# Optimization experiments

Hardware: AMD Instinct MI355X
Metric: run time of the kernel (lower is better)

The kernel has to match this reference:

```python
import math
from itertools import product
import jax, jax.numpy as jnp
import numpy as np

# ---- static config (mirrors LPD.__init__) ----
IMG_W, IMG_H = 1920, 1080
MIN_SIZES = [[10, 16, 24], [32, 48], [64, 96], [128, 192, 256]]
STEPS = [8, 16, 32, 64]
VARIANCE = (0.1, 0.2)
CONF_THR = 0.3
NMS_THR = 0.3
TOP_K = 2000
KEEP_TOP_K = 750
BATCH = 16


def make_priors() -> np.ndarray:
    """Anchor grid in normalized (cx, cy, w, h), kornia _PriorBox order:
    per level, per cell (row-major), per min_size."""
    levels = []
    for step, mss in zip(STEPS, MIN_SIZES):
        fh, fw = math.ceil(IMG_H / step), math.ceil(IMG_W / step)
        ii, jj = np.meshgrid(np.arange(fh), np.arange(fw), indexing='ij')
        cx = (jj + 0.5) * step / IMG_W  # [fh, fw]
        cy = (ii + 0.5) * step / IMG_H
        nms_ = len(mss)
        cx = np.broadcast_to(cx[..., None], (fh, fw, nms_))
        cy = np.broadcast_to(cy[..., None], (fh, fw, nms_))
        skx = np.broadcast_to(np.array(mss, np.float64) / IMG_W, (fh, fw, nms_))
        sky = np.broadcast_to(np.array(mss, np.float64) / IMG_H, (fh, fw, nms_))
        levels.append(np.stack([cx, cy, skx, sky], -1).reshape(-1, 4))
    return np.concatenate(levels, 0).astype(np.float32)  # [N, 4]

N_PRIORS = make_priors().shape[0]  # 119130 for 1920x1080


def decode(loc, priors):
    """loc [B,N,14], priors [N,4] -> scaled [B,N,14] (x1y1x2y2 + 5 landmarks)."""
    var = jnp.asarray(VARIANCE, loc.dtype)
    p_xy, p_wh = priors[:, :2], priors[:, 2:4]
    cxcy = p_xy + loc[..., 0:2] * VARIANCE[0] * p_wh
    wh = p_wh * jnp.exp(loc[..., 2:4] * var)
    x1y1 = cxcy - wh * 0.5
    x2y2 = x1y1 + wh
    # 5 landmark points
    lmk = p_xy[None, :, None, :] + loc[..., 4:14].reshape(*loc.shape[:-1], 5, 2) * VARIANCE[0] * p_wh[None, :, None, :]
    boxes = jnp.concatenate([x1y1, x2y2, lmk.reshape(*loc.shape[:-1], 10)], -1)
    scale = jnp.tile(jnp.asarray([IMG_W, IMG_H], loc.dtype), 7)
    return boxes * scale


def nms_keep(b, s):
    """Greedy NMS. b [K,4] sorted by descending score s [K]. Returns bool keep [K]."""
    area = jnp.clip(b[:, 2] - b[:, 0], 0.0) * jnp.clip(b[:, 3] - b[:, 1], 0.0)
    lt = jnp.maximum(b[:, None, :2], b[None, :, :2])
    rb = jnp.minimum(b[:, None, 2:4], b[None, :, 2:4])
    whi = jnp.clip(rb - lt, 0.0)
    inter = whi[..., 0] * whi[..., 1]
    iou_m = inter / (area[:, None] + area[None, :] - inter + 1e-9)  # [K,K]
    K = b.shape[0]
    idx = jnp.arange(K)

    def step(active, i):
        keep_i = active[i]
        active = active & ~(keep_i & (iou_m[i] > NMS_THR) & (idx > i))
        return active, keep_i

    _, keep = jax.lax.scan(step, s > 0.0, idx)
    return keep


def setup_inputs() -> dict:
    key = jax.random.key(0)
    k1, k2, k3 = jax.random.split(key, 3)
    return {
        'loc': jax.random.normal(k1, (BATCH, N_PRIORS, 14), jnp.float32),
        'conf': jax.random.normal(k2, (BATCH, N_PRIORS, 2), jnp.float32),
        'iou': jax.random.normal(k3, (BATCH, N_PRIORS, 1), jnp.float32),
    }


def reference(loc, conf, iou):
    priors = jnp.asarray(make_priors())  # [N,4] constant
    cls = jax.nn.softmax(conf, axis=-1)[..., 1]          # [B,N]
    iou_s = jnp.clip(iou[..., 0], 0.0, 1.0)
    scores = jnp.sqrt(cls * iou_s)
    scores = jnp.where(scores >= CONF_THR, scores, 0.0)  # confidence threshold
    boxes = decode(loc, priors)                          # [B,N,14]
    top_s, top_i = jax.lax.top_k(scores, TOP_K)          # sorted desc
    boxes_k = jnp.take_along_axis(boxes, top_i[..., None], axis=1)  # [B,K,14]
    keep = jax.vmap(nms_keep)(boxes_k[..., :4], top_s)   # [B,K] bool
    keep = keep & (jnp.cumsum(keep.astype(jnp.int32), axis=-1) <= KEEP_TOP_K)
    dets = jnp.concatenate([boxes_k, (top_s * keep)[..., None]], -1)  # [B,K,15]
    return dets
```

## Files before the change

### kernel.cpp

```cpp
#include <hip/hip_runtime.h>
#include <math.h>

#define BB 16
#define TOPK 2000
#define KEEPK 750
#define CAND_CAP 4096
#define EDGE_CAP 8192
#define HIST_BINS 256
#define BIN_BASE 0x3E99u

#define OFF_HIST   0
#define OFF_CCOUNT 16384
#define OFF_ECOUNT 16448
#define ZERO_BYTES 16512
#define OFF_SBITS  16512

__global__ __launch_bounds__(256) void k_scores(const float* __restrict__ conf,
                                                const float* __restrict__ iou,
                                                unsigned* __restrict__ sbits,
                                                unsigned* __restrict__ hist, int N) {
  __shared__ unsigned h[HIST_BINS];
  int b = blockIdx.y;
  for (int i = threadIdx.x; i < HIST_BINS; i += blockDim.x) h[i] = 0;
  __syncthreads();
  const float2* c2 = (const float2*)conf + (size_t)b * N;
  const float* iu = iou + (size_t)b * N;
  unsigned* sb = sbits + (size_t)b * N;
  int n0 = blockIdx.x * 4096;
#pragma unroll 4
  for (int k = 0; k < 16; ++k) {
    int n = n0 + k * 256 + threadIdx.x;
    if (n < N) {
      float2 c = c2[n];
      float m = fmaxf(c.x, c.y);
      float e0 = (float)exp((double)(c.x - m));
      float e1 = (float)exp((double)(c.y - m));
      float p1 = e1 / (e0 + e1);
      float ic = fminf(fmaxf(iu[n], 0.0f), 1.0f);
      float s = sqrtf(p1 * ic);
      s = (s >= 0.3f) ? s : 0.0f;
      unsigned bits = __float_as_uint(s);
      sb[n] = bits;
      if (bits != 0u) {
        int bin = (int)(bits >> 16) - (int)BIN_BASE;
        bin = bin < 0 ? 0 : (bin > 255 ? 255 : bin);
        atomicAdd(&h[bin], 1u);
      }
    }
  }
  __syncthreads();
  for (int i = threadIdx.x; i < HIST_BINS; i += blockDim.x)
    if (h[i]) atomicAdd(&hist[b * HIST_BINS + i], h[i]);
}

__global__ __launch_bounds__(256) void k_compact(const unsigned* __restrict__ sbits,
                                                 const unsigned* __restrict__ hist,
                                                 unsigned* __restrict__ ccount,
                                                 unsigned long long* __restrict__ ckeys,
                                                 int N) {
  __shared__ unsigned sT;
  __shared__ unsigned long long masks[32];
  __shared__ unsigned wioff[32];
  __shared__ unsigned blockbase;
  int b = blockIdx.y;
  int tid = threadIdx.x, lane = tid & 63, wv = tid >> 6;

  if (tid < 64) {
    const unsigned* h = hist + b * HIST_BINS;
    unsigned v0 = h[255 - (4 * lane + 0)];
    unsigned v1 = h[255 - (4 * lane + 1)];
    unsigned v2 = h[255 - (4 * lane + 2)];
    unsigned v3 = h[255 - (4 * lane + 3)];
    unsigned p0 = v0, p1 = p0 + v1, p2 = p1 + v2, p3 = p2 + v3;
    unsigned tot = p3, pre = tot;
    for (int off = 1; off < 64; off <<= 1) {
      unsigned q = __shfl_up(pre, off);
      if (lane >= off) pre += q;
    }
    unsigned excl = pre - tot;
    int kk = -1;
    if (excl + p0 >= TOPK) kk = 0;
    else if (excl + p1 >= TOPK) kk = 1;
    else if (excl + p2 >= TOPK) kk = 2;
    else if (excl + p3 >= TOPK) kk = 3;
    unsigned long long m = __ballot(kk >= 0);
    int bin = 0;
    if (m != 0ull) {
      int fl = __ffsll((unsigned long long)m) - 1;
      int fk = __shfl(kk, fl);
      bin = 255 - (4 * fl + fk);
    }
    if (lane == 0) sT = ((unsigned)(BIN_BASE + (unsigned)bin)) << 16;
  }
  __syncthreads();
  unsigned T = sT;

  const unsigned* sb = sbits + (size_t)b * N;
  int n0 = blockIdx.x * 2048;
  unsigned v[8];
  unsigned long long mk[8];
#pragma unroll
  for (int k = 0; k < 8; ++k) {
    int n = n0 + k * 256 + tid;
    v[k] = (n < N) ? sb[n] : 0u;
    bool p = v[k] >= T;
    mk[k] = __ballot(p);
    if (lane == 0) masks[k * 4 + wv] = mk[k];
  }
  __syncthreads();
  if (tid < 64) {
    unsigned c = (tid < 32) ? (unsigned)__popcll(masks[tid]) : 0u;
    unsigned pre = c;
    for (int off = 1; off < 64; off <<= 1) {
      unsigned q = __shfl_up(pre, off);
      if (lane >= off) pre += q;
    }
    if (tid < 32) wioff[tid] = pre - c;
    if (tid == 31) blockbase = atomicAdd(&ccount[b], pre);
  }
  __syncthreads();
  unsigned base = blockbase;
#pragma unroll
  for (int k = 0; k < 8; ++k) {
    if ((mk[k] >> lane) & 1ull) {
      unsigned pos = base + wioff[k * 4 + wv] +
                     (unsigned)__popcll(mk[k] & ((1ull << lane) - 1ull));
      if (pos < CAND_CAP) {
        int n = n0 + k * 256 + tid;
        ckeys[(size_t)b * CAND_CAP + pos] =
            ((unsigned long long)v[k] << 32) | (unsigned)(~(unsigned)n);
      }
    }
  }
}

__global__ __launch_bounds__(1024) void k_sort(const unsigned* __restrict__ ccount,
                                               const unsigned long long* __restrict__ ckeys,
                                               float* __restrict__ top_s,
                                               unsigned* __restrict__ top_i) {
  __shared__ unsigned long long s[CAND_CAP];
  int b = blockIdx.x;
  unsigned c = ccount[b];
  if (c > CAND_CAP) c = CAND_CAP;
  for (int i = threadIdx.x; i < CAND_CAP; i += 1024)
    s[i] = (i < (int)c) ? ckeys[(size_t)b * CAND_CAP + i] : 0ull;
  __syncthreads();
  for (int k = 2; k <= CAND_CAP; k <<= 1) {
    for (int j = k >> 1; j > 0; j >>= 1) {
      for (int i = threadIdx.x; i < CAND_CAP; i += 1024) {
        int p = i ^ j;
        if (p > i) {
          bool up = (i & k) == 0;
          unsigned long long a = s[i], bb2 = s[p];
          bool sw = up ? (a < bb2) : (a > bb2);
          if (sw) { s[i] = bb2; s[p] = a; }
        }
      }
      __syncthreads();
    }
  }
  for (int r = threadIdx.x; r < TOPK; r += 1024) {
    unsigned long long key = s[r];
    top_s[b * TOPK + r] = __uint_as_float((unsigned)(key >> 32));
    top_i[b * TOPK + r] = ~(unsigned)key;
  }
}

__global__ __launch_bounds__(256) void k_decode(const float* __restrict__ loc,
                                                const unsigned* __restrict__ top_i,
                                                float* __restrict__ out,
                                                float4* __restrict__ boxes4, int N) {
  int r = blockIdx.x * blockDim.x + threadIdx.x;
  int b = blockIdx.y;
  if (r >= TOPK) return;
  unsigned idxu = top_i[b * TOPK + r];
  if (idxu >= (unsigned)N) idxu = 0;
  int i = (int)idxu;
  int off, fw, st, nm, lvl;
  if (i < 97200)       { lvl = 0; off = 0;      fw = 240; st = 8;  nm = 3; }
  else if (i < 113520) { lvl = 1; off = 97200;  fw = 120; st = 16; nm = 2; }
  else if (i < 117600) { lvl = 2; off = 113520; fw = 60;  st = 32; nm = 2; }
  else                 { lvl = 3; off = 117600; fw = 30;  st = 64; nm = 3; }
  int t = i - off;
  int cell = t / nm;
  int k = t - cell * nm;
  int row = cell / fw;
  int col = cell - row * fw;
  int msv = (lvl == 0) ? (k == 0 ? 10 : (k == 1 ? 16 : 24))
          : (lvl == 1) ? (k == 0 ? 32 : 48)
          : (lvl == 2) ? (k == 0 ? 64 : 96)
                       : (k == 0 ? 128 : (k == 1 ? 192 : 256));
  float cx  = (float)(((double)col + 0.5) * (double)st / 1920.0);
  float cy  = (float)(((double)row + 0.5) * (double)st / 1080.0);
  float skx = (float)((double)msv / 1920.0);
  float sky = (float)((double)msv / 1080.0);
  const float2* lp2 = (const float2*)(loc + ((size_t)b * N + (size_t)i) * 14);
  float l[14];
#pragma unroll
  for (int q = 0; q < 7; ++q) { float2 v = lp2[q]; l[2 * q] = v.x; l[2 * q + 1] = v.y; }
  float cx2 = cx + (l[0] * 0.1f) * skx;
  float cy2 = cy + (l[1] * 0.1f) * sky;
  float wx = skx * expf(l[2] * 0.1f);
  float wy = sky * expf(l[3] * 0.2f);
  float x1 = cx2 - wx * 0.5f, y1 = cy2 - wy * 0.5f;
  float x2 = x1 + wx, y2 = y1 + wy;
  float X1 = x1 * 1920.0f, Y1 = y1 * 1080.0f, X2 = x2 * 1920.0f, Y2 = y2 * 1080.0f;
  float* o = out + ((size_t)b * TOPK + r) * 15;
  o[0] = X1; o[1] = Y1; o[2] = X2; o[3] = Y2;
#pragma unroll
  for (int q = 0; q < 5; ++q) {
    o[4 + 2 * q] = (cx + (l[4 + 2 * q] * 0.1f) * skx) * 1920.0f;
    o[5 + 2 * q] = (cy + (l[5 + 2 * q] * 0.1f) * sky) * 1080.0f;
  }
  boxes4[b * TOPK + r] = make_float4(X1, Y1, X2, Y2);
}

__global__ __launch_bounds__(256) void k_edges(const float4* __restrict__ boxes4,
                                               unsigned* __restrict__ ecount,
                                               unsigned* __restrict__ edges) {
  __shared__ float4 cb[256];
  __shared__ unsigned loc_e[1024];
  __shared__ unsigned lcnt, gbase;
  int b = blockIdx.y;
  int t = blockIdx.x;
  int ib = 0;
  while ((ib + 1) * (ib + 2) / 2 <= t) ++ib;
  int jb = t - ib * (ib + 1) / 2;
  int tid = threadIdx.x;
  if (tid == 0) lcnt = 0;
  int j0 = jb * 256;
  {
    int j = j0 + tid;
    cb[tid] = (j < TOPK) ? boxes4[b * TOPK + j]
                         : make_float4(-1e30f, -1e30f, -1e30f, -1e30f);
  }
  __syncthreads();
  int r = ib * 256 + tid;
  bool valid = r < TOPK;
  float4 A = valid ? boxes4[b * TOPK + r] : make_float4(0, 0, 0, 0);
  float areaA = fmaxf(A.z - A.x, 0.f) * fmaxf(A.w - A.y, 0.f);
  int cmax = r - j0;
  if (cmax > 256) cmax = 256;
  if (!valid) cmax = 0;
  for (int c = 0; c < cmax; ++c) {
    float4 Bx = cb[c];
    float xx1 = fmaxf(A.x, Bx.x), yy1 = fmaxf(A.y, Bx.y);
    float xx2 = fminf(A.z, Bx.z), yy2 = fminf(A.w, Bx.w);
    float w = fmaxf(xx2 - xx1, 0.f), hgt = fmaxf(yy2 - yy1, 0.f);
    float inter = w * hgt;
    float areaB = fmaxf(Bx.z - Bx.x, 0.f) * fmaxf(Bx.w - Bx.y, 0.f);
    float iouv = inter / (areaA + areaB - inter + 1e-9f);
    if (iouv > 0.3f) {
      unsigned p = atomicAdd(&lcnt, 1u);
      if (p < 1024u) loc_e[p] = ((unsigned)r << 16) | (unsigned)(j0 + c);
    }
  }
  __syncthreads();
  unsigned cnt = lcnt;
  if (cnt > 1024u) cnt = 1024u;
  if (tid == 0 && cnt) gbase = atomicAdd(&ecount[b], cnt);
  __syncthreads();
  if (cnt)
    for (unsigned e = tid; e < cnt; e += 256) {
      unsigned p = gbase + e;
      if (p < EDGE_CAP) edges[b * EDGE_CAP + p] = loc_e[e];
    }
}

__global__ __launch_bounds__(256) void k_nms(const float* __restrict__ top_s,
                                             const unsigned* __restrict__ ecount,
                                             const unsigned* __restrict__ edges,
                                             float* __restrict__ out) {
  int b = blockIdx.x;
  __shared__ unsigned long long A[32], K[32], S[32];
  __shared__ unsigned pref[32];
  __shared__ unsigned ecache[2048];
  __shared__ int changed;
  int tid = threadIdx.x, lane = tid & 63, wv = tid >> 6;
  for (int base = 0; base < 2048; base += 256) {
    int i = base + tid;
    bool act = (i < TOPK) && (top_s[b * TOPK + i] > 0.0f);
    unsigned long long m = __ballot(act);
    if (lane == 0) { int w = (base >> 6) + wv; A[w] = m; K[w] = m; }
  }
  unsigned E = ecount[b];
  if (E > EDGE_CAP) E = EDGE_CAP;
  unsigned Ec = E > 2048u ? 2048u : E;
  for (unsigned e = tid; e < Ec; e += 256) ecache[e] = edges[b * EDGE_CAP + e];
  __syncthreads();
  for (int it = 0; it < 32; ++it) {
    if (tid == 0) changed = 0;
    if (tid < 32) S[tid] = 0ull;
    __syncthreads();
    for (unsigned e = tid; e < Ec; e += 256) {
      unsigned v = ecache[e];
      unsigned i = v >> 16, j = v & 0xFFFFu;
      if ((K[j >> 6] >> (j & 63)) & 1ull) atomicOr(&S[i >> 6], 1ull << (i & 63));
    }
    for (unsigned e = 2048u + tid; e < E; e += 256) {
      unsigned v = edges[b * EDGE_CAP + e];
      unsigned i = v >> 16, j = v & 0xFFFFu;
      if ((K[j >> 6] >> (j & 63)) & 1ull) atomicOr(&S[i >> 6], 1ull << (i & 63));
    }
    __syncthreads();
    if (tid < 32) {
      unsigned long long nk = A[tid] & ~S[tid];
      if (nk != K[tid]) { K[tid] = nk; changed = 1; }
    }
    __syncthreads();
    if (!changed) break;
  }
  if (tid == 0) {
    unsigned acc = 0;
    for (int w = 0; w < 32; ++w) { pref[w] = acc; acc += (unsigned)__popcll(K[w]); }
  }
  __syncthreads();
  for (int base = 0; base < 2048; base += 256) {
    int i = base + tid;
    if (i < TOPK) {
      int w = i >> 6;
      unsigned long long bit = (K[w] >> (i & 63)) & 1ull;
      unsigned rank = pref[w] + (unsigned)__popcll(K[w] & ((1ull << (i & 63)) - 1ull)) +
                      (unsigned)bit;
      float sv = top_s[b * TOPK + i];
      out[((size_t)b * TOPK + i) * 15 + 14] = (bit && rank <= KEEPK) ? sv : 0.0f;
    }
  }
}

extern "C" void kernel_launch(void* const* d_in, const int* in_sizes, int n_in,
                              void* d_out, int out_size, void* d_ws, size_t ws_size,
                              hipStream_t stream) {
  const float* loc  = (const float*)d_in[0];
  const float* conf = (const float*)d_in[1];
  const float* iou  = (const float*)d_in[2];
  float* out = (float*)d_out;
  int N = in_sizes[2] / BB;

  char* ws = (char*)d_ws;
  unsigned* hist   = (unsigned*)(ws + OFF_HIST);
  unsigned* ccount = (unsigned*)(ws + OFF_CCOUNT);
  unsigned* ecount = (unsigned*)(ws + OFF_ECOUNT);
  unsigned* sbits  = (unsigned*)(ws + OFF_SBITS);
  size_t off = (size_t)OFF_SBITS + (size_t)BB * N * 4;
  off = (off + 15) & ~(size_t)15;
  unsigned long long* ckeys = (unsigned long long*)(ws + off); off += (size_t)BB * CAND_CAP * 8;
  float*    top_s = (float*)(ws + off);    off += (size_t)BB * TOPK * 4;
  unsigned* top_i = (unsigned*)(ws + off); off += (size_t)BB * TOPK * 4;
  off = (off + 15) & ~(size_t)15;
  float4* boxes4 = (float4*)(ws + off);    off += (size_t)BB * TOPK * 16;
  unsigned* edges = (unsigned*)(ws + off); off += (size_t)BB * EDGE_CAP * 4;

  hipMemsetAsync(ws, 0, ZERO_BYTES, stream);

  k_scores<<<dim3((N + 4095) / 4096, BB), 256, 0, stream>>>(conf, iou, sbits, hist, N);
  k_compact<<<dim3((N + 2047) / 2048, BB), 256, 0, stream>>>(sbits, hist, ccount, ckeys, N);
  k_sort<<<BB, 1024, 0, stream>>>(ccount, ckeys, top_s, top_i);
  k_decode<<<dim3((TOPK + 255) / 256, BB), 256, 0, stream>>>(loc, top_i, out, boxes4, N);
  k_edges<<<dim3(36, BB), 256, 0, stream>>>(boxes4, ecount, edges);
  k_nms<<<BB, 256, 0, stream>>>(top_s, ecount, edges, out);
}
```

Measured before the change: 296.8 us.

## Register-resident bitonic sort with wavefront shuffles, fused with box decode

Rewrites the per-batch bitonic sort so each thread holds four keys in registers. In-thread compares handle strides below 4 and wavefront XOR shuffles handle strides up to 64 wide in thread space, so shared memory and block barriers are used only for the large strides. The decode step is fused into the sort kernel, which removes one kernel launch and the top_i round trip through global memory. In exchange, decode now runs on only 500 threads per batch across 16 blocks, so the gathers from loc are less parallel.

```diff
diff --git a/kernel.cpp b/kernel.cpp
--- a/kernel.cpp
+++ b/kernel.cpp
@@ -134,85 +134,115 @@
   }
 }
 
-__global__ __launch_bounds__(1024) void k_sort(const unsigned* __restrict__ ccount,
-                                               const unsigned long long* __restrict__ ckeys,
-                                               float* __restrict__ top_s,
-                                               unsigned* __restrict__ top_i) {
+__global__ __launch_bounds__(1024) void k_sort_decode(
+    const unsigned* __restrict__ ccount, const unsigned long long* __restrict__ ckeys,
+    const float* __restrict__ loc, float* __restrict__ top_s,
+    float* __restrict__ out, float4* __restrict__ boxes4, int N) {
   __shared__ unsigned long long s[CAND_CAP];
   int b = blockIdx.x;
+  int t = threadIdx.x;
   unsigned c = ccount[b];
   if (c > CAND_CAP) c = CAND_CAP;
-  for (int i = threadIdx.x; i < CAND_CAP; i += 1024)
-    s[i] = (i < (int)c) ? ckeys[(size_t)b * CAND_CAP + i] : 0ull;
-  __syncthreads();
+  const unsigned long long* src = ckeys + (size_t)b * CAND_CAP;
+  unsigned long long key[4];
+#pragma unroll
+  for (int e = 0; e < 4; ++e) {
+    int i = 4 * t + e;
+    key[e] = (i < (int)c) ? src[i] : 0ull;
+  }
   for (int k = 2; k <= CAND_CAP; k <<= 1) {
     for (int j = k >> 1; j > 0; j >>= 1) {
-      for (int i = threadIdx.x; i < CAND_CAP; i += 1024) {
-        int p = i ^ j;
-        if (p > i) {
-          bool up = (i & k) == 0;
-          unsigned long long a = s[i], bb2 = s[p];
-          bool sw = up ? (a < bb2) : (a > bb2);
-          if (sw) { s[i] = bb2; s[p] = a; }
+      if (j >= 256) {
+        __syncthreads();
+#pragma unroll
+        for (int e = 0; e < 4; ++e) s[4 * t + e] = key[e];
+        __syncthreads();
+        int pbase = (4 * t) ^ j;
+        bool own_lo = ((4 * t) & j) == 0;
+        bool dir = ((4 * t) & k) == 0;
+        bool keep_max = (own_lo == dir);
+#pragma unroll
+        for (int e = 0; e < 4; ++e) {
+          unsigned long long o = s[pbase + e];
+          unsigned long long mx = key[e] > o ? key[e] : o;
+          unsigned long long mn = key[e] > o ? o : key[e];
+          key[e] = keep_max ? mx : mn;
+        }
+      } else if (j >= 4) {
+        int d = j >> 2;
+        bool own_lo = (t & d) == 0;
+        bool dir = ((4 * t) & k) == 0;
+        bool keep_max = (own_lo == dir);
+#pragma unroll
+        for (int e = 0; e < 4; ++e) {
+          unsigned long long o = __shfl_xor(key[e], d, 64);
+          unsigned long long mx = key[e] > o ? key[e] : o;
+          unsigned long long mn = key[e] > o ? o : key[e];
+          key[e] = keep_max ? mx : mn;
+        }
+      } else {
+#pragma unroll
+        for (int e = 0; e < 4; ++e) {
+          int p = e ^ j;
+          if (p > e) {
+            int i = 4 * t + e;
+            bool dir = ((i & k) == 0);
+            bool need = dir ? (key[e] < key[p]) : (key[e] > key[p]);
+            if (need) { unsigned long long tmp = key[e]; key[e] = key[p]; key[p] = tmp; }
+          }
         }
       }
-      __syncthreads();
-    }
-  }
-  for (int r = threadIdx.x; r < TOPK; r += 1024) {
-    unsigned long long key = s[r];
-    top_s[b * TOPK + r] = __uint_as_float((unsigned)(key >> 32));
-    top_i[b * TOPK + r] = ~(unsigned)key;
-  }
-}
-
-__global__ __launch_bounds__(256) void k_decode(const float* __restrict__ loc,
-                                                const unsigned* __restrict__ top_i,
-                                                float* __restrict__ out,
-                                                float4* __restrict__ boxes4, int N) {
-  int r = blockIdx.x * blockDim.x + threadIdx.x;
-  int b = blockIdx.y;
-  if (r >= TOPK) return;
-  unsigned idxu = top_i[b * TOPK + r];
-  if (idxu >= (unsigned)N) idxu = 0;
-  int i = (int)idxu;
-  int off, fw, st, nm, lvl;
-  if (i < 97200)       { lvl = 0; off = 0;      fw = 240; st = 8;  nm = 3; }
-  else if (i < 113520) { lvl = 1; off = 97200;  fw = 120; st = 16; nm = 2; }
-  else if (i < 117600) { lvl = 2; off = 113520; fw = 60;  st = 32; nm = 2; }
-  else                 { lvl = 3; off = 117600; fw = 30;  st = 64; nm = 3; }
-  int t = i - off;
-  int cell = t / nm;
-  int k = t - cell * nm;
-  int row = cell / fw;
-  int col = cell - row * fw;
-  int msv = (lvl == 0) ? (k == 0 ? 10 : (k == 1 ? 16 : 24))
-          : (lvl == 1) ? (k == 0 ? 32 : 48)
-          : (lvl == 2) ? (k == 0 ? 64 : 96)
-                       : (k == 0 ? 128 : (k == 1 ? 192 : 256));
-  float cx  = (float)(((double)col + 0.5) * (double)st / 1920.0);
-  float cy  = (float)(((double)row + 0.5) * (double)st / 1080.0);
-  float skx = (float)((double)msv / 1920.0);
-  float sky = (float)((double)msv / 1080.0);
-  const float2* lp2 = (const float2*)(loc + ((size_t)b * N + (size_t)i) * 14);
-  float l[14];
-#pragma unroll
-  for (int q = 0; q < 7; ++q) { float2 v = lp2[q]; l[2 * q] = v.x; l[2 * q + 1] = v.y; }
-  float cx2 = cx + (l[0] * 0.1f) * skx;
-  float cy2 = cy + (l[1] * 0.1f) * sky;
-  float wx = skx * expf(l[2] * 0.1f);
-  float wy = sky * expf(l[3] * 0.2f);
-  float x1 = cx2 - wx * 0.5f, y1 = cy2 - wy * 0.5f;
-  float x2 = x1 + wx, y2 = y1 + wy;
-  float X1 = x1 * 1920.0f, Y1 = y1 * 1080.0f, X2 = x2 * 1920.0f, Y2 = y2 * 1080.0f;
-  float* o = out + ((size_t)b * TOPK + r) * 15;
-  o[0] = X1; o[1] = Y1; o[2] = X2; o[3] = Y2;
-#pragma unroll
-  for (int q = 0; q < 5; ++q) {
-    o[4 + 2 * q] = (cx + (l[4 + 2 * q] * 0.1f) * skx) * 1920.0f;
-    o[5 + 2 * q] = (cy + (l[5 + 2 * q] * 0.1f) * sky) * 1080.0f;
-  }
-  boxes4[b * TOPK + r] = make_float4(X1, Y1, X2, Y2);
+    }
+  }
+  if (t < TOPK / 4) {
+#pragma unroll
+    for (int e = 0; e < 4; ++e) {
+      int r = 4 * t + e;
+      unsigned long long kk = key[e];
+      float sv = __uint_as_float((unsigned)(kk >> 32));
+      top_s[b * TOPK + r] = sv;
+      unsigned idxu = ~(unsigned)kk;
+      if (idxu >= (unsigned)N) idxu = 0;
+      int i = (int)idxu;
+      int off, fw, st, nm, lvl;
+      if (i < 97200)       { lvl = 0; off = 0;      fw = 240; st = 8;  nm = 3; }
+      else if (i < 113520) { lvl = 1; off = 97200;  fw = 120; st = 16; nm = 2; }
+      else if (i < 117600) { lvl = 2; off = 113520; fw = 60;  st = 32; nm = 2; }
+      else                 { lvl = 3; off = 117600; fw = 30;  st = 64; nm = 3; }
+      int tt = i - off;
+      int cell = tt / nm;
+      int kms = tt - cell * nm;
+      int row = cell / fw;
+      int col = cell - row * fw;
+      int msv = (lvl == 0) ? (kms == 0 ? 10 : (kms == 1 ? 16 : 24))
+              : (lvl == 1) ? (kms == 0 ? 32 : 48)
+              : (lvl == 2) ? (kms == 0 ? 64 : 96)
+                           : (kms == 0 ? 128 : (kms == 1 ? 192 : 256));
+      float cx  = (float)(((double)col + 0.5) * (double)st / 1920.0);
+      float cy  = (float)(((double)row + 0.5) * (double)st / 1080.0);
+      float skx = (float)((double)msv / 1920.0);
+      float sky = (float)((double)msv / 1080.0);
+      const float2* lp2 = (const float2*)(loc + ((size_t)b * N + (size_t)i) * 14);
+      float l[14];
+#pragma unroll
+      for (int q = 0; q < 7; ++q) { float2 v = lp2[q]; l[2 * q] = v.x; l[2 * q + 1] = v.y; }
+      float cx2 = cx + (l[0] * 0.1f) * skx;
+      float cy2 = cy + (l[1] * 0.1f) * sky;
+      float wx = skx * expf(l[2] * 0.1f);
+      float wy = sky * expf(l[3] * 0.2f);
+      float x1 = cx2 - wx * 0.5f, y1 = cy2 - wy * 0.5f;
+      float x2 = x1 + wx, y2 = y1 + wy;
+      float X1 = x1 * 1920.0f, Y1 = y1 * 1080.0f, X2 = x2 * 1920.0f, Y2 = y2 * 1080.0f;
+      float* o = out + ((size_t)b * TOPK + r) * 15;
+      o[0] = X1; o[1] = Y1; o[2] = X2; o[3] = Y2;
+#pragma unroll
+      for (int q = 0; q < 5; ++q) {
+        o[4 + 2 * q] = (cx + (l[4 + 2 * q] * 0.1f) * skx) * 1920.0f;
+        o[5 + 2 * q] = (cy + (l[5 + 2 * q] * 0.1f) * sky) * 1080.0f;
+      }
+      boxes4[b * TOPK + r] = make_float4(X1, Y1, X2, Y2);
+    }
+  }
 }
 
 __global__ __launch_bounds__(256) void k_edges(const float4* __restrict__ boxes4,
@@ -345,8 +375,7 @@
   size_t off = (size_t)OFF_SBITS + (size_t)BB * N * 4;
   off = (off + 15) & ~(size_t)15;
   unsigned long long* ckeys = (unsigned long long*)(ws + off); off += (size_t)BB * CAND_CAP * 8;
-  float*    top_s = (float*)(ws + off);    off += (size_t)BB * TOPK * 4;
-  unsigned* top_i = (unsigned*)(ws + off); off += (size_t)BB * TOPK * 4;
+  float* top_s = (float*)(ws + off);       off += (size_t)BB * TOPK * 4;
   off = (off + 15) & ~(size_t)15;
   float4* boxes4 = (float4*)(ws + off);    off += (size_t)BB * TOPK * 16;
   unsigned* edges = (unsigned*)(ws + off); off += (size_t)BB * EDGE_CAP * 4;
@@ -355,8 +384,7 @@
 
   k_scores<<<dim3((N + 4095) / 4096, BB), 256, 0, stream>>>(conf, iou, sbits, hist, N);
   k_compact<<<dim3((N + 2047) / 2048, BB), 256, 0, stream>>>(sbits, hist, ccount, ckeys, N);
-  k_sort<<<BB, 1024, 0, stream>>>(ccount, ckeys, top_s, top_i);
-  k_decode<<<dim3((TOPK + 255) / 256, BB), 256, 0, stream>>>(loc, top_i, out, boxes4, N);
+  k_sort_decode<<<BB, 1024, 0, stream>>>(ccount, ckeys, loc, top_s, out, boxes4, N);
   k_edges<<<dim3(36, BB), 256, 0, stream>>>(boxes4, ecount, edges);
   k_nms<<<BB, 256, 0, stream>>>(top_s, ecount, edges, out);
 }
```

Result: no change. 293.8 us (-1.0%).
